# Kernel optimization log

Hardware: AMD Instinct MI355X
Metric: run time of the kernel (lower is better)

## Reference

```python
import jax, jax.numpy as jnp
import numpy as np

B = 16384
N_DENSE = 13
N_SPARSE = 26
ONEHOT_DIM = 1000          # feat_onehot_dim for every sparse feature
K = 8                      # FFM latent dim
FIELD_NUM = N_DENSE + N_SPARSE            # 39
FEATURE_NUM = N_DENSE + N_SPARSE * ONEHOT_DIM  # 26013


def setup_inputs() -> dict:
    key = jax.random.key(0)
    k1, k2, k3, k4 = jax.random.split(key, 4)
    dense_x = jax.random.normal(k1, (B, N_DENSE), dtype=jnp.float32)
    sparse_x = jax.random.randint(k2, (B, N_SPARSE), 0, ONEHOT_DIM, dtype=jnp.int32)
    # linear layer weight (flattened [feature_num] row vector) and bias
    W = jax.random.normal(k3, (FEATURE_NUM,), dtype=jnp.float32) * 0.01
    b = jnp.zeros((1,), dtype=jnp.float32)
    # FFM latent tensor v: [feature_num, field_num, k]
    v = jax.random.normal(k4, (FEATURE_NUM, FIELD_NUM, K), dtype=jnp.float32) * 0.02
    return {"dense_x": dense_x, "sparse_x": sparse_x, "W": W, "b": b, "v": v}


def reference(dense_x, sparse_x, W, b, v):
    # Global one-hot column index for each sparse field:
    # feature i occupies rows [13 + i*1000, 13 + (i+1)*1000) of the one-hot x.
    offsets = N_DENSE + jnp.arange(N_SPARSE, dtype=sparse_x.dtype) * ONEHOT_DIM
    idx = sparse_x + offsets[None, :]                     # [B, 26]

    # linear part: x @ W + b, exploiting one-hot sparsity of x
    linear = dense_x @ W[:N_DENSE] + jnp.sum(W[idx], axis=1) + b[0]  # [B]

    # field_f = x @ v  (tensordot over feature dim), again via gather
    field_f = (jnp.einsum('bd,dgk->bgk', dense_x, v[:N_DENSE])
               + jnp.sum(v[idx], axis=1))                 # [B, 39, 8]

    # sum_{i<j} <f_i, f_j> = 0.5 * ((sum_g f_g)^2 - sum_g f_g^2), summed over k
    s = jnp.sum(field_f, axis=1)                          # [B, 8]
    sq = jnp.sum(field_f * field_f, axis=1)               # [B, 8]
    inter = 0.5 * jnp.sum(s * s - sq, axis=-1)            # [B]

    return jax.nn.sigmoid(linear + inter)                 # [B]
```

## Files before the change

### kernel.cpp

```cpp
#include <hip/hip_runtime.h>


constexpr int ND     = 13;
constexpr int NS     = 26;
constexpr int OH     = 1000;
constexpr int GK4    = 78;
constexpr int ROWB   = 1248;
constexpr int NROWSV = 26013;
constexpr int BSTRIDE= 640;

__global__ __launch_bounds__(256) void cvt_bf16(
    const float4* __restrict__ vin,
    char*         __restrict__ ws)
{
    const int tid = (int)(blockIdx.x * 256 + threadIdx.x);
    if (tid >= NROWSV * GK4) return;
    const int row = tid / GK4;
    const int p   = tid - row * GK4;
    const float4 f = vin[tid];
    auto rne = [](float x) -> unsigned {
        unsigned u = __float_as_uint(x);
        return (u + 0x7FFFu + ((u >> 16) & 1u)) >> 16;
    };
    uint2 o;
    o.x = rne(f.x) | (rne(f.y) << 16);
    o.y = rne(f.z) | (rne(f.w) << 16);
    *reinterpret_cast<uint2*>(ws + (size_t)row * BSTRIDE + (p << 3)) = o;
}

__global__ __launch_bounds__(256, 4) void ffm_fwd_b(
    const float* __restrict__ dense_x,
    const int*   __restrict__ sparse_x,
    const float* __restrict__ W,
    const float* __restrict__ bias,
    const float* __restrict__ v,
    const char*  __restrict__ wsb,
    float*       __restrict__ out,
    int nrows)
{
    const int lane = (int)(threadIdx.x & 63u);
    const int row  = (int)(blockIdx.x * 4 + (threadIdx.x >> 6));
    if (row >= nrows) return;

    const float4* __restrict__ v4 = reinterpret_cast<const float4*>(v);

    const bool  act1  = lane < (GK4 - 64);
    const int   slot2 = 64 + (act1 ? lane : 13);
    const float fm1   = act1 ? 1.f : 0.f;

    int   myidx = 0;
    float myx   = 0.f;
    if (lane < NS) myidx = sparse_x[row * NS + lane] + ND + lane * OH;
    if (lane < ND) myx   = dense_x[row * ND + lane];

    float lin = 0.f;
    if (lane < NS) lin = W[myidx];
    if (lane < ND) lin = fmaf(myx, W[lane], lin);

    float a0x=0.f,a0y=0.f,a0z=0.f,a0w=0.f;
    float a1x=0.f,a1y=0.f,a1z=0.f,a1w=0.f;

    #pragma unroll
    for (int d = 0; d < ND; ++d) {
        const float x  = __int_as_float(__builtin_amdgcn_readlane(__float_as_int(myx), d));
        const float xm = x * fm1;
        const float4 p0 = v4[d * GK4 + lane];
        const float4 p1 = v4[d * GK4 + slot2];
        a0x = fmaf(x,  p0.x, a0x); a0y = fmaf(x,  p0.y, a0y);
        a0z = fmaf(x,  p0.z, a0z); a0w = fmaf(x,  p0.w, a0w);
        a1x = fmaf(xm, p1.x, a1x); a1y = fmaf(xm, p1.y, a1y);
        a1z = fmaf(xm, p1.z, a1z); a1w = fmaf(xm, p1.w, a1w);
    }

    const int   lane14 = lane / 14;
    const int   lanej  = lane - lane14 * 14;
    const float fmT    = (lane < 56) ? 1.f : 0.f;
    const float fmT6   = (lane < 28) ? 1.f : 0.f;

    auto mainLoad = [&](int r) -> uint2 {
        const int idx = __builtin_amdgcn_readlane(myidx, r);
        return *reinterpret_cast<const uint2*>(
            wsb + (size_t)(unsigned)idx * BSTRIDE + (lane << 3));
    };
    auto tailLoad = [&](int g) -> uint2 {
        int src = 4 * g + lane14;
        src = src > (NS - 1) ? (NS - 1) : src;
        const int idx = __shfl(myidx, src);
        return *reinterpret_cast<const uint2*>(
            wsb + (size_t)(unsigned)idx * BSTRIDE + 512 + (lanej << 3));
    };
    auto lo16 = [](unsigned u) -> float { return __uint_as_float(u << 16); };
    auto hi16 = [](unsigned u) -> float { return __uint_as_float(u & 0xFFFF0000u); };

    uint2 m[6], t[2];
    #pragma unroll
    for (int r = 0; r < 6; ++r) m[r] = mainLoad(r);
    t[0] = tailLoad(0);
    t[1] = tailLoad(1);
    __builtin_amdgcn_sched_barrier(0);

    #pragma unroll
    for (int r = 0; r < NS; ++r) {
        const uint2 q = m[r % 6];
        a0x += lo16(q.x); a0y += hi16(q.x);
        a0z += lo16(q.y); a0w += hi16(q.y);
        if (r + 6 < NS) m[r % 6] = mainLoad(r + 6);
        if ((r & 3) == 0) {
            const int g = r >> 2;
            const float fm = (g == 6) ? fmT6 : fmT;
            const uint2 qt = t[g & 1];
            a1x = fmaf(fm, lo16(qt.x), a1x); a1y = fmaf(fm, hi16(qt.x), a1y);
            a1z = fmaf(fm, lo16(qt.y), a1z); a1w = fmaf(fm, hi16(qt.y), a1w);
            if (g + 2 <= 6) t[g & 1] = tailLoad(g + 2);
        }
        __builtin_amdgcn_sched_barrier(0);
    }

    {
        const float fmc = (lane < 14) ? 1.f : 0.f;
        float bx = a1x + __shfl(a1x, lane + 14) + __shfl(a1x, lane + 28) + __shfl(a1x, lane + 42);
        float by = a1y + __shfl(a1y, lane + 14) + __shfl(a1y, lane + 28) + __shfl(a1y, lane + 42);
        float bz = a1z + __shfl(a1z, lane + 14) + __shfl(a1z, lane + 28) + __shfl(a1z, lane + 42);
        float bw = a1w + __shfl(a1w, lane + 14) + __shfl(a1w, lane + 28) + __shfl(a1w, lane + 42);
        a1x = bx * fmc; a1y = by * fmc; a1z = bz * fmc; a1w = bw * fmc;
    }

    float sx = a0x + a1x, sy = a0y + a1y, sz = a0z + a1z, sw = a0w + a1w;
    float qx = fmaf(a0x, a0x, a1x * a1x);
    float qy = fmaf(a0y, a0y, a1y * a1y);
    float qz = fmaf(a0z, a0z, a1z * a1z);
    float qw = fmaf(a0w, a0w, a1w * a1w);

    #pragma unroll
    for (int mk = 2; mk <= 32; mk <<= 1) {
        sx += __shfl_xor(sx, mk); sy += __shfl_xor(sy, mk);
        sz += __shfl_xor(sz, mk); sw += __shfl_xor(sw, mk);
        qx += __shfl_xor(qx, mk); qy += __shfl_xor(qy, mk);
        qz += __shfl_xor(qz, mk); qw += __shfl_xor(qw, mk);
    }
    float val = (sx * sx - qx) + (sy * sy - qy) + (sz * sz - qz) + (sw * sw - qw);
    val += __shfl_xor(val, 1);

    #pragma unroll
    for (int mk = 1; mk <= 32; mk <<= 1) lin += __shfl_xor(lin, mk);

    if (lane == 0) {
        const float tt = lin + bias[0] + 0.5f * val;
        out[row] = 1.f / (1.f + __expf(-tt));
    }
}

__global__ __launch_bounds__(256, 4) void ffm_fwd_f32(
    const float* __restrict__ dense_x, const int* __restrict__ sparse_x,
    const float* __restrict__ W, const float* __restrict__ bias,
    const float* __restrict__ v, float* __restrict__ out, int nrows)
{
    const int lane = (int)(threadIdx.x & 63u);
    const int row  = (int)(blockIdx.x * 4 + (threadIdx.x >> 6));
    if (row >= nrows) return;
    const float4* __restrict__ v4 = reinterpret_cast<const float4*>(v);
    const char*   __restrict__ vb = reinterpret_cast<const char*>(v);
    const bool  act1  = lane < (GK4 - 64);
    const int   slot2 = 64 + (act1 ? lane : 13);
    const float fm1   = act1 ? 1.f : 0.f;
    int   myidx = 0; float myx = 0.f;
    if (lane < NS) myidx = sparse_x[row * NS + lane] + ND + lane * OH;
    if (lane < ND) myx   = dense_x[row * ND + lane];
    float lin = 0.f;
    if (lane < NS) lin = W[myidx];
    if (lane < ND) lin = fmaf(myx, W[lane], lin);
    float a0x=0.f,a0y=0.f,a0z=0.f,a0w=0.f, a1x=0.f,a1y=0.f,a1z=0.f,a1w=0.f;
    #pragma unroll
    for (int d = 0; d < ND; ++d) {
        const float x  = __int_as_float(__builtin_amdgcn_readlane(__float_as_int(myx), d));
        const float xm = x * fm1;
        const float4 p0 = v4[d * GK4 + lane];
        const float4 p1 = v4[d * GK4 + slot2];
        a0x = fmaf(x,p0.x,a0x); a0y = fmaf(x,p0.y,a0y);
        a0z = fmaf(x,p0.z,a0z); a0w = fmaf(x,p0.w,a0w);
        a1x = fmaf(xm,p1.x,a1x); a1y = fmaf(xm,p1.y,a1y);
        a1z = fmaf(xm,p1.z,a1z); a1w = fmaf(xm,p1.w,a1w);
    }
    const int lane14 = lane / 14, lanej = lane - lane14 * 14;
    const float fmT = (lane < 56) ? 1.f : 0.f, fmT6 = (lane < 28) ? 1.f : 0.f;
    auto mainLoad = [&](int r) -> float4 {
        const int idx = __builtin_amdgcn_readlane(myidx, r);
        return reinterpret_cast<const float4*>(vb + (size_t)(unsigned)idx * ROWB)[lane];
    };
    auto tailLoad = [&](int g) -> float4 {
        int src = 4 * g + lane14; src = src > (NS-1) ? (NS-1) : src;
        const int idx = __shfl(myidx, src);
        return *reinterpret_cast<const float4*>(vb + (size_t)(unsigned)idx * ROWB + 1024 + (lanej << 4));
    };
    float4 m[6], t[2];
    #pragma unroll
    for (int r = 0; r < 6; ++r) m[r] = mainLoad(r);
    t[0] = tailLoad(0); t[1] = tailLoad(1);
    __builtin_amdgcn_sched_barrier(0);
    #pragma unroll
    for (int r = 0; r < NS; ++r) {
        const float4 p0 = m[r % 6];
        a0x += p0.x; a0y += p0.y; a0z += p0.z; a0w += p0.w;
        if (r + 6 < NS) m[r % 6] = mainLoad(r + 6);
        if ((r & 3) == 0) {
            const int g = r >> 2;
            const float fm = (g == 6) ? fmT6 : fmT;
            const float4 p1 = t[g & 1];
            a1x = fmaf(fm,p1.x,a1x); a1y = fmaf(fm,p1.y,a1y);
            a1z = fmaf(fm,p1.z,a1z); a1w = fmaf(fm,p1.w,a1w);
            if (g + 2 <= 6) t[g & 1] = tailLoad(g + 2);
        }
        __builtin_amdgcn_sched_barrier(0);
    }
    {
        const float fmc = (lane < 14) ? 1.f : 0.f;
        float bx = a1x + __shfl(a1x,lane+14) + __shfl(a1x,lane+28) + __shfl(a1x,lane+42);
        float by = a1y + __shfl(a1y,lane+14) + __shfl(a1y,lane+28) + __shfl(a1y,lane+42);
        float bz = a1z + __shfl(a1z,lane+14) + __shfl(a1z,lane+28) + __shfl(a1z,lane+42);
        float bw = a1w + __shfl(a1w,lane+14) + __shfl(a1w,lane+28) + __shfl(a1w,lane+42);
        a1x = bx*fmc; a1y = by*fmc; a1z = bz*fmc; a1w = bw*fmc;
    }
    float sx=a0x+a1x, sy=a0y+a1y, sz=a0z+a1z, sw=a0w+a1w;
    float qx=fmaf(a0x,a0x,a1x*a1x), qy=fmaf(a0y,a0y,a1y*a1y);
    float qz=fmaf(a0z,a0z,a1z*a1z), qw=fmaf(a0w,a0w,a1w*a1w);
    #pragma unroll
    for (int mk = 2; mk <= 32; mk <<= 1) {
        sx += __shfl_xor(sx,mk); sy += __shfl_xor(sy,mk);
        sz += __shfl_xor(sz,mk); sw += __shfl_xor(sw,mk);
        qx += __shfl_xor(qx,mk); qy += __shfl_xor(qy,mk);
        qz += __shfl_xor(qz,mk); qw += __shfl_xor(qw,mk);
    }
    float val = (sx*sx-qx) + (sy*sy-qy) + (sz*sz-qz) + (sw*sw-qw);
    val += __shfl_xor(val, 1);
    #pragma unroll
    for (int mk = 1; mk <= 32; mk <<= 1) lin += __shfl_xor(lin, mk);
    if (lane == 0) {
        const float tt = lin + bias[0] + 0.5f * val;
        out[row] = 1.f / (1.f + __expf(-tt));
    }
}

extern "C" void kernel_launch(void* const* d_in, const int* in_sizes, int n_in,
                              void* d_out, int out_size, void* d_ws, size_t ws_size,
                              hipStream_t stream) {
    const float* dense_x  = (const float*)d_in[0];
    const int*   sparse_x = (const int*)d_in[1];
    const float* W        = (const float*)d_in[2];
    const float* bias     = (const float*)d_in[3];
    const float* v        = (const float*)d_in[4];
    float*       out      = (float*)d_out;

    const int nrows  = in_sizes[0] / ND;
    const int blocks = (nrows + 3) / 4;

    const size_t need = (size_t)NROWSV * BSTRIDE;
    if (ws_size >= need) {
        const int ncvt = NROWSV * GK4;
        hipLaunchKernelGGL(cvt_bf16, dim3((ncvt + 255) / 256), dim3(256), 0, stream,
                           reinterpret_cast<const float4*>(v), (char*)d_ws);
        hipLaunchKernelGGL(ffm_fwd_b, dim3(blocks), dim3(256), 0, stream,
                           dense_x, sparse_x, W, bias, v, (const char*)d_ws, out, nrows);
    } else {
        hipLaunchKernelGGL(ffm_fwd_f32, dim3(blocks), dim3(256), 0, stream,
                           dense_x, sparse_x, W, bias, v, out, nrows);
    }
}
```

Before: 120.0 us.

## Map one field per lane with 16-byte bf16 loads, dropping tail split

```diff
diff --git a/kernel.cpp b/kernel.cpp
--- a/kernel.cpp
+++ b/kernel.cpp
@@ -8,32 +8,35 @@
 constexpr int ROWB   = 1248;
 constexpr int NROWSV = 26013;
 constexpr int BSTRIDE= 640;
+constexpr int NL     = 39;
 
 __global__ __launch_bounds__(256) void cvt_bf16(
     const float4* __restrict__ vin,
     char*         __restrict__ ws)
 {
     const int tid = (int)(blockIdx.x * 256 + threadIdx.x);
-    if (tid >= NROWSV * GK4) return;
-    const int row = tid / GK4;
-    const int p   = tid - row * GK4;
-    const float4 f = vin[tid];
+    if (tid >= NROWSV * NL) return;
+    const int row = tid / NL;
+    const int p   = tid - row * NL;
+    const float4 f0 = vin[2 * tid];
+    const float4 f1 = vin[2 * tid + 1];
     auto rne = [](float x) -> unsigned {
         unsigned u = __float_as_uint(x);
         return (u + 0x7FFFu + ((u >> 16) & 1u)) >> 16;
     };
-    uint2 o;
-    o.x = rne(f.x) | (rne(f.y) << 16);
-    o.y = rne(f.z) | (rne(f.w) << 16);
-    *reinterpret_cast<uint2*>(ws + (size_t)row * BSTRIDE + (p << 3)) = o;
-}
-
-__global__ __launch_bounds__(256, 4) void ffm_fwd_b(
+    uint4 o;
+    o.x = rne(f0.x) | (rne(f0.y) << 16);
+    o.y = rne(f0.z) | (rne(f0.w) << 16);
+    o.z = rne(f1.x) | (rne(f1.y) << 16);
+    o.w = rne(f1.z) | (rne(f1.w) << 16);
+    *reinterpret_cast<uint4*>(ws + (size_t)row * BSTRIDE + ((size_t)p << 4)) = o;
+}
+
+__global__ __launch_bounds__(256, 4) void ffm_fwd_c(
     const float* __restrict__ dense_x,
     const int*   __restrict__ sparse_x,
     const float* __restrict__ W,
     const float* __restrict__ bias,
-    const float* __restrict__ v,
     const char*  __restrict__ wsb,
     float*       __restrict__ out,
     int nrows)
@@ -42,11 +45,9 @@
     const int row  = (int)(blockIdx.x * 4 + (threadIdx.x >> 6));
     if (row >= nrows) return;
 
-    const float4* __restrict__ v4 = reinterpret_cast<const float4*>(v);
-
-    const bool  act1  = lane < (GK4 - 64);
-    const int   slot2 = 64 + (act1 ? lane : 13);
-    const float fm1   = act1 ? 1.f : 0.f;
+    const int   g  = lane < NL ? lane : (NL - 1);
+    const float fm = lane < NL ? 1.f : 0.f;
+    const size_t goff = (size_t)g << 4;
 
     int   myidx = 0;
     float myx   = 0.f;
@@ -57,92 +58,63 @@
     if (lane < NS) lin = W[myidx];
     if (lane < ND) lin = fmaf(myx, W[lane], lin);
 
-    float a0x=0.f,a0y=0.f,a0z=0.f,a0w=0.f;
-    float a1x=0.f,a1y=0.f,a1z=0.f,a1w=0.f;
-
-    #pragma unroll
-    for (int d = 0; d < ND; ++d) {
-        const float x  = __int_as_float(__builtin_amdgcn_readlane(__float_as_int(myx), d));
-        const float xm = x * fm1;
-        const float4 p0 = v4[d * GK4 + lane];
-        const float4 p1 = v4[d * GK4 + slot2];
-        a0x = fmaf(x,  p0.x, a0x); a0y = fmaf(x,  p0.y, a0y);
-        a0z = fmaf(x,  p0.z, a0z); a0w = fmaf(x,  p0.w, a0w);
-        a1x = fmaf(xm, p1.x, a1x); a1y = fmaf(xm, p1.y, a1y);
-        a1z = fmaf(xm, p1.z, a1z); a1w = fmaf(xm, p1.w, a1w);
-    }
-
-    const int   lane14 = lane / 14;
-    const int   lanej  = lane - lane14 * 14;
-    const float fmT    = (lane < 56) ? 1.f : 0.f;
-    const float fmT6   = (lane < 28) ? 1.f : 0.f;
-
-    auto mainLoad = [&](int r) -> uint2 {
-        const int idx = __builtin_amdgcn_readlane(myidx, r);
-        return *reinterpret_cast<const uint2*>(
-            wsb + (size_t)(unsigned)idx * BSTRIDE + (lane << 3));
-    };
-    auto tailLoad = [&](int g) -> uint2 {
-        int src = 4 * g + lane14;
-        src = src > (NS - 1) ? (NS - 1) : src;
-        const int idx = __shfl(myidx, src);
-        return *reinterpret_cast<const uint2*>(
-            wsb + (size_t)(unsigned)idx * BSTRIDE + 512 + (lanej << 3));
-    };
     auto lo16 = [](unsigned u) -> float { return __uint_as_float(u << 16); };
     auto hi16 = [](unsigned u) -> float { return __uint_as_float(u & 0xFFFF0000u); };
 
-    uint2 m[6], t[2];
+    float a[8];
+    #pragma unroll
+    for (int j = 0; j < 8; ++j) a[j] = 0.f;
+
+    #pragma unroll
+    for (int d = 0; d < ND; ++d) {
+        const float x = __int_as_float(__builtin_amdgcn_readlane(__float_as_int(myx), d));
+        const uint4 q = *reinterpret_cast<const uint4*>(wsb + (size_t)d * BSTRIDE + goff);
+        a[0] = fmaf(x, lo16(q.x), a[0]); a[1] = fmaf(x, hi16(q.x), a[1]);
+        a[2] = fmaf(x, lo16(q.y), a[2]); a[3] = fmaf(x, hi16(q.y), a[3]);
+        a[4] = fmaf(x, lo16(q.z), a[4]); a[5] = fmaf(x, hi16(q.z), a[5]);
+        a[6] = fmaf(x, lo16(q.w), a[6]); a[7] = fmaf(x, hi16(q.w), a[7]);
+    }
+
+    auto mainLoad = [&](int r) -> uint4 {
+        const int idx = __builtin_amdgcn_readlane(myidx, r);
+        return *reinterpret_cast<const uint4*>(
+            wsb + (size_t)(unsigned)idx * BSTRIDE + goff);
+    };
+
+    uint4 m[6];
     #pragma unroll
     for (int r = 0; r < 6; ++r) m[r] = mainLoad(r);
-    t[0] = tailLoad(0);
-    t[1] = tailLoad(1);
     __builtin_amdgcn_sched_barrier(0);
 
     #pragma unroll
     for (int r = 0; r < NS; ++r) {
-        const uint2 q = m[r % 6];
-        a0x += lo16(q.x); a0y += hi16(q.x);
-        a0z += lo16(q.y); a0w += hi16(q.y);
+        const uint4 q = m[r % 6];
+        a[0] += lo16(q.x); a[1] += hi16(q.x);
+        a[2] += lo16(q.y); a[3] += hi16(q.y);
+        a[4] += lo16(q.z); a[5] += hi16(q.z);
+        a[6] += lo16(q.w); a[7] += hi16(q.w);
         if (r + 6 < NS) m[r % 6] = mainLoad(r + 6);
-        if ((r & 3) == 0) {
-            const int g = r >> 2;
-            const float fm = (g == 6) ? fmT6 : fmT;
-            const uint2 qt = t[g & 1];
-            a1x = fmaf(fm, lo16(qt.x), a1x); a1y = fmaf(fm, hi16(qt.x), a1y);
-            a1z = fmaf(fm, lo16(qt.y), a1z); a1w = fmaf(fm, hi16(qt.y), a1w);
-            if (g + 2 <= 6) t[g & 1] = tailLoad(g + 2);
-        }
         __builtin_amdgcn_sched_barrier(0);
     }
 
-    {
-        const float fmc = (lane < 14) ? 1.f : 0.f;
-        float bx = a1x + __shfl(a1x, lane + 14) + __shfl(a1x, lane + 28) + __shfl(a1x, lane + 42);
-        float by = a1y + __shfl(a1y, lane + 14) + __shfl(a1y, lane + 28) + __shfl(a1y, lane + 42);
-        float bz = a1z + __shfl(a1z, lane + 14) + __shfl(a1z, lane + 28) + __shfl(a1z, lane + 42);
-        float bw = a1w + __shfl(a1w, lane + 14) + __shfl(a1w, lane + 28) + __shfl(a1w, lane + 42);
-        a1x = bx * fmc; a1y = by * fmc; a1z = bz * fmc; a1w = bw * fmc;
-    }
-
-    float sx = a0x + a1x, sy = a0y + a1y, sz = a0z + a1z, sw = a0w + a1w;
-    float qx = fmaf(a0x, a0x, a1x * a1x);
-    float qy = fmaf(a0y, a0y, a1y * a1y);
-    float qz = fmaf(a0z, a0z, a1z * a1z);
-    float qw = fmaf(a0w, a0w, a1w * a1w);
-
-    #pragma unroll
-    for (int mk = 2; mk <= 32; mk <<= 1) {
-        sx += __shfl_xor(sx, mk); sy += __shfl_xor(sy, mk);
-        sz += __shfl_xor(sz, mk); sw += __shfl_xor(sw, mk);
-        qx += __shfl_xor(qx, mk); qy += __shfl_xor(qy, mk);
-        qz += __shfl_xor(qz, mk); qw += __shfl_xor(qw, mk);
-    }
-    float val = (sx * sx - qx) + (sy * sy - qy) + (sz * sz - qz) + (sw * sw - qw);
-    val += __shfl_xor(val, 1);
-
-    #pragma unroll
-    for (int mk = 1; mk <= 32; mk <<= 1) lin += __shfl_xor(lin, mk);
+    float s[8];
+    float qtot = 0.f;
+    #pragma unroll
+    for (int j = 0; j < 8; ++j) {
+        const float aj = a[j] * fm;
+        s[j] = aj;
+        qtot = fmaf(aj, aj, qtot);
+    }
+    #pragma unroll
+    for (int mk = 1; mk <= 32; mk <<= 1) {
+        #pragma unroll
+        for (int j = 0; j < 8; ++j) s[j] += __shfl_xor(s[j], mk);
+        qtot += __shfl_xor(qtot, mk);
+        lin  += __shfl_xor(lin, mk);
+    }
+    float val = -qtot;
+    #pragma unroll
+    for (int j = 0; j < 8; ++j) val = fmaf(s[j], s[j], val);
 
     if (lane == 0) {
         const float tt = lin + bias[0] + 0.5f * val;
@@ -160,7 +132,7 @@
     if (row >= nrows) return;
     const float4* __restrict__ v4 = reinterpret_cast<const float4*>(v);
     const char*   __restrict__ vb = reinterpret_cast<const char*>(v);
-    const bool  act1  = lane < (GK4 - 64);
+    const bool  act1  = lane < 14;
     const int   slot2 = 64 + (act1 ? lane : 13);
     const float fm1   = act1 ? 1.f : 0.f;
     int   myidx = 0; float myx = 0.f;
@@ -187,8 +159,8 @@
         const int idx = __builtin_amdgcn_readlane(myidx, r);
         return reinterpret_cast<const float4*>(vb + (size_t)(unsigned)idx * ROWB)[lane];
     };
-    auto tailLoad = [&](int g) -> float4 {
-        int src = 4 * g + lane14; src = src > (NS-1) ? (NS-1) : src;
+    auto tailLoad = [&](int g2) -> float4 {
+        int src = 4 * g2 + lane14; src = src > (NS-1) ? (NS-1) : src;
         const int idx = __shfl(myidx, src);
         return *reinterpret_cast<const float4*>(vb + (size_t)(unsigned)idx * ROWB + 1024 + (lanej << 4));
     };
@@ -203,12 +175,12 @@
         a0x += p0.x; a0y += p0.y; a0z += p0.z; a0w += p0.w;
         if (r + 6 < NS) m[r % 6] = mainLoad(r + 6);
         if ((r & 3) == 0) {
-            const int g = r >> 2;
-            const float fm = (g == 6) ? fmT6 : fmT;
-            const float4 p1 = t[g & 1];
-            a1x = fmaf(fm,p1.x,a1x); a1y = fmaf(fm,p1.y,a1y);
-            a1z = fmaf(fm,p1.z,a1z); a1w = fmaf(fm,p1.w,a1w);
-            if (g + 2 <= 6) t[g & 1] = tailLoad(g + 2);
+            const int g2 = r >> 2;
+            const float fmv = (g2 == 6) ? fmT6 : fmT;
+            const float4 p1 = t[g2 & 1];
+            a1x = fmaf(fmv,p1.x,a1x); a1y = fmaf(fmv,p1.y,a1y);
+            a1z = fmaf(fmv,p1.z,a1z); a1w = fmaf(fmv,p1.w,a1w);
+            if (g2 + 2 <= 6) t[g2 & 1] = tailLoad(g2 + 2);
         }
         __builtin_amdgcn_sched_barrier(0);
     }
@@ -255,11 +227,11 @@
 
     const size_t need = (size_t)NROWSV * BSTRIDE;
     if (ws_size >= need) {
-        const int ncvt = NROWSV * GK4;
+        const int ncvt = NROWSV * NL;
         hipLaunchKernelGGL(cvt_bf16, dim3((ncvt + 255) / 256), dim3(256), 0, stream,
                            reinterpret_cast<const float4*>(v), (char*)d_ws);
-        hipLaunchKernelGGL(ffm_fwd_b, dim3(blocks), dim3(256), 0, stream,
-                           dense_x, sparse_x, W, bias, v, (const char*)d_ws, out, nrows);
+        hipLaunchKernelGGL(ffm_fwd_c, dim3(blocks), dim3(256), 0, stream,
+                           dense_x, sparse_x, W, bias, (const char*)d_ws, out, nrows);
     } else {
         hipLaunchKernelGGL(ffm_fwd_f32, dim3(blocks), dim3(256), 0, stream,
                            dense_x, sparse_x, W, bias, v, out, nrows);
```

Measured after the change: 115.3 us. -3.9%, faster.
